# Kernel optimization log

Hardware: AMD Instinct MI355X
Metric: run time of the kernel (lower is better)

The kernel has to match this reference:

```python
import jax, jax.numpy as jnp
import numpy as np

N_ATOMS = 1000
BOX_L = 30.0      # cubic cell edge (Angstrom)
MAX_CUTOFF = 8.0  # max(cutoff)


def _np_cart(a, b, c):
    # numpy equivalent of torch.cartesian_prod for 3 1-D arrays
    g = np.meshgrid(a, b, c, indexing='ij')
    return np.stack(g, axis=-1).reshape(-1, 3)


def _np_get_shifts(cell, cutoff):
    # mirrors TorchNeighborListRangeSeparated._get_shifts (pbc=True on all axes)
    recip = np.linalg.inv(cell).T
    inv_len = np.linalg.norm(recip, axis=1)
    nrep = np.ceil(cutoff * inv_len).astype(np.int64)
    r1 = np.arange(1, nrep[0] + 1, dtype=np.float64)
    r2 = np.arange(1, nrep[1] + 1, dtype=np.float64)
    r3 = np.arange(1, nrep[2] + 1, dtype=np.float64)
    o = np.zeros(1, dtype=np.float64)
    return np.concatenate([
        _np_cart(r1, r2, r3), _np_cart(r1, r2, o), _np_cart(r1, r2, -r3),
        _np_cart(r1, o, r3), _np_cart(r1, o, o), _np_cart(r1, o, -r3),
        _np_cart(r1, -r2, r3), _np_cart(r1, -r2, o), _np_cart(r1, -r2, -r3),
        _np_cart(o, r2, r3), _np_cart(o, r2, o), _np_cart(o, r2, -r3),
        _np_cart(o, o, r3)], axis=0)


def setup_inputs() -> dict:
    key = jax.random.key(0)
    cell_np = np.eye(3) * BOX_L
    shifts = jnp.asarray(_np_get_shifts(cell_np, MAX_CUTOFF), dtype=jnp.float32)  # [13,3]
    positions = jax.random.uniform(key, (N_ATOMS, 3), dtype=jnp.float32) * BOX_L
    return {
        "positions": positions,
        "cell": jnp.asarray(cell_np, dtype=jnp.float32),
        "shifts": shifts,
        "cutoffs": jnp.array([4.0, 8.0], dtype=jnp.float32),
    }


def reference(positions, cell, shifts, cutoffs):
    """PBC-aware pairwise distance^2 + per-cutoff neighbor masks.

    Returns:
      d2:    [P] squared distances over all candidate pairs
             (N*(N-1)/2 in-cell pairs followed by S*N*N shifted-image pairs)
      masks: [n_cutoffs, P] int32 in-cutoff indicator (d2 < cutoff^2)
    """
    n = positions.shape[0]
    # in-cell pairs (torch.combinations -> i<j)
    iu, ju = jnp.triu_indices(n, k=1)
    rij_c = positions[iu] - positions[ju]                       # [Pc,3]
    d2_c = jnp.sum(rij_c * rij_c, axis=-1)                      # [Pc]
    # shifted-image pairs: all (shift, i, j)
    shift_values = shifts @ cell                                # [S,3]
    rij_o = (positions[None, :, None, :] - positions[None, None, :, :]
             + shift_values[:, None, None, :])                  # [S,N,N,3]
    d2_o = jnp.sum(rij_o * rij_o, axis=-1).reshape(-1)          # [S*N*N]
    d2 = jnp.concatenate([d2_c, d2_o], axis=0)                  # [P]
    masks = (d2[None, :] < (cutoffs ** 2)[:, None]).astype(jnp.int32)
    return d2, masks
```

## Files before the change

kernel.cpp:

```cpp
#include <hip/hip_runtime.h>
#include <math.h>


typedef float f32x4 __attribute__((ext_vector_type(4)));

template <int NCUT>
__global__ void __launch_bounds__(256) nbr_fast(
    const float* __restrict__ pos,
    const float* __restrict__ cell,
    const float* __restrict__ shifts,
    const float* __restrict__ cutoffs,
    int n, int S,
    float* __restrict__ out, unsigned P, unsigned Pc)
{
    const int tid = threadIdx.x;
    const int s   = blockIdx.z;

    double cut2[NCUT];
#pragma unroll
    for (int c = 0; c < NCUT; ++c) {
        double cv = (double)cutoffs[c];
        cut2[c] = cv * cv;
    }

    if (s < S) {
        const unsigned j0 = (unsigned)tid << 2;
        if (j0 >= (unsigned)n) return;
        const unsigned i = blockIdx.y;

        double s0 = (double)shifts[3*s+0], s1 = (double)shifts[3*s+1], s2 = (double)shifts[3*s+2];
        double sv0 = s0 * (double)cell[0] + s1 * (double)cell[3] + s2 * (double)cell[6];
        double sv1 = s0 * (double)cell[1] + s1 * (double)cell[4] + s2 * (double)cell[7];
        double sv2 = s0 * (double)cell[2] + s1 * (double)cell[5] + s2 * (double)cell[8];
        double pix = (double)pos[3*i+0];
        double piy = (double)pos[3*i+1];
        double piz = (double)pos[3*i+2];

        const float4* pj = (const float4*)(pos + 3 * j0);
        float4 a = pj[0], b = pj[1], c4 = pj[2];
        float jx[4] = {a.x, a.w, b.z, c4.y};
        float jy[4] = {a.y, b.x, b.w, c4.z};
        float jz[4] = {a.z, b.y, c4.x, c4.w};

        f32x4 d2v;
        f32x4 mv[NCUT];
#pragma unroll
        for (int k = 0; k < 4; ++k) {
            double dx = (pix - (double)jx[k]) + sv0;
            double dy = (piy - (double)jy[k]) + sv1;
            double dz = (piz - (double)jz[k]) + sv2;
            double d2 = dx*dx + dy*dy + dz*dz;
            d2v[k] = (float)d2;
#pragma unroll
            for (int c = 0; c < NCUT; ++c) mv[c][k] = (d2 < cut2[c]) ? 1.0f : 0.0f;
        }

        const unsigned t0 = ((unsigned)s * (unsigned)n + i) * (unsigned)n + j0 + Pc;
        *(f32x4*)(out + t0) = d2v;
#pragma unroll
        for (int c = 0; c < NCUT; ++c)
            *(f32x4*)(out + (unsigned)(c + 1) * P + t0) = mv[c];
    } else {
        const unsigned p0 = ((blockIdx.y * 256u) + (unsigned)tid) << 2;
        if (p0 >= Pc) return;

        const long long tn = 2LL * n - 1;
        f32x4 d2v;
        f32x4 mv[NCUT];
#pragma unroll
        for (int k = 0; k < 4; ++k) {
            long long p = (long long)p0 + k;
            double D = (double)(tn * tn) - 8.0 * (double)p;
            long long i = (long long)(((double)tn - sqrt(D)) * 0.5);
            if (i < 0) i = 0;
            if (i > n - 2) i = n - 2;
            while ((i + 1) * (tn - (i + 1)) / 2 <= p) ++i;
            while (i * (tn - i) / 2 > p) --i;
            long long j = p - i * (tn - i) / 2 + i + 1;

            double dx = (double)pos[3*i+0] - (double)pos[3*j+0];
            double dy = (double)pos[3*i+1] - (double)pos[3*j+1];
            double dz = (double)pos[3*i+2] - (double)pos[3*j+2];
            double d2 = dx*dx + dy*dy + dz*dz;
            d2v[k] = (float)d2;
#pragma unroll
            for (int c = 0; c < NCUT; ++c) mv[c][k] = (d2 < cut2[c]) ? 1.0f : 0.0f;
        }

        *(f32x4*)(out + p0) = d2v;
#pragma unroll
        for (int c = 0; c < NCUT; ++c)
            *(f32x4*)(out + (unsigned)(c + 1) * P + p0) = mv[c];
    }
}

__global__ void __launch_bounds__(256) nbr_scalar(
    const float* __restrict__ pos,
    const float* __restrict__ cell,
    const float* __restrict__ shifts,
    const float* __restrict__ cutoffs,
    int ncut, int n,
    float* __restrict__ out, long long P, long long Pc)
{
    long long p = (long long)blockIdx.x * 256 + threadIdx.x;
    if (p >= P) return;

    double d2;
    if (p >= Pc) {
        long long q = p - Pc;
        unsigned long long nn = (unsigned long long)n * n;
        unsigned s = (unsigned)(q / nn);
        unsigned long long r = q - (unsigned long long)s * nn;
        unsigned i = (unsigned)(r / n);
        unsigned j = (unsigned)(r - (unsigned long long)i * n);
        double s0 = (double)shifts[3*s+0], s1 = (double)shifts[3*s+1], s2 = (double)shifts[3*s+2];
        double sv0 = s0*(double)cell[0] + s1*(double)cell[3] + s2*(double)cell[6];
        double sv1 = s0*(double)cell[1] + s1*(double)cell[4] + s2*(double)cell[7];
        double sv2 = s0*(double)cell[2] + s1*(double)cell[5] + s2*(double)cell[8];
        double dx = ((double)pos[3*i+0] - (double)pos[3*j+0]) + sv0;
        double dy = ((double)pos[3*i+1] - (double)pos[3*j+1]) + sv1;
        double dz = ((double)pos[3*i+2] - (double)pos[3*j+2]) + sv2;
        d2 = dx*dx + dy*dy + dz*dz;
    } else {
        long long tn = 2LL * n - 1;
        double D = (double)(tn * tn) - 8.0 * (double)p;
        long long i = (long long)(((double)tn - sqrt(D)) * 0.5);
        if (i < 0) i = 0;
        if (i > n - 2) i = n - 2;
        while ((i + 1) * (tn - (i + 1)) / 2 <= p) ++i;
        while (i * (tn - i) / 2 > p) --i;
        long long j = p - i * (tn - i) / 2 + i + 1;
        double dx = (double)pos[3*i+0] - (double)pos[3*j+0];
        double dy = (double)pos[3*i+1] - (double)pos[3*j+1];
        double dz = (double)pos[3*i+2] - (double)pos[3*j+2];
        d2 = dx*dx + dy*dy + dz*dz;
    }
    out[p] = (float)d2;
    for (int c = 0; c < ncut; ++c) {
        double cv = (double)cutoffs[c];
        out[(long long)(c + 1) * P + p] = (d2 < cv * cv) ? 1.0f : 0.0f;
    }
}

extern "C" void kernel_launch(void* const* d_in, const int* in_sizes, int n_in,
                              void* d_out, int out_size, void* d_ws, size_t ws_size,
                              hipStream_t stream)
{
    const float* pos     = (const float*)d_in[0];
    const float* cell    = (const float*)d_in[1];
    const float* shifts  = (const float*)d_in[2];
    const float* cutoffs = (const float*)d_in[3];
    int n    = in_sizes[0] / 3;
    int S    = in_sizes[2] / 3;
    int ncut = in_sizes[3];

    long long Pc = (long long)n * (n - 1) / 2;
    long long P  = Pc + (long long)S * n * n;
    float* out = (float*)d_out;

    bool fast = ((n & 3) == 0) && (n <= 2049) && (ncut >= 1) && (ncut <= 4) &&
                (3 * P < (1LL << 31));
    if (fast) {
        dim3 grid(1, n, S + 1);
        unsigned uP = (unsigned)P, uPc = (unsigned)Pc;
        switch (ncut) {
        case 1: nbr_fast<1><<<grid, 256, 0, stream>>>(pos, cell, shifts, cutoffs, n, S, out, uP, uPc); break;
        case 2: nbr_fast<2><<<grid, 256, 0, stream>>>(pos, cell, shifts, cutoffs, n, S, out, uP, uPc); break;
        case 3: nbr_fast<3><<<grid, 256, 0, stream>>>(pos, cell, shifts, cutoffs, n, S, out, uP, uPc); break;
        default: nbr_fast<4><<<grid, 256, 0, stream>>>(pos, cell, shifts, cutoffs, n, S, out, uP, uPc); break;
        }
    } else {
        int blocks = (int)((P + 255) / 256);
        nbr_scalar<<<blocks, 256, 0, stream>>>(pos, cell, shifts, cutoffs,
                                               ncut, n, out, P, Pc);
    }
}
```

Baseline: 170.9 us.

## Replace 3D per-row grid with flat grid-stride loop over output chunks

Drops the grid of one block per (shift, i) row, where only part of each 256-thread block had work. Instead a fixed grid of up to 2048 blocks walks all 4-element output chunks with a grid-stride loop. Each chunk recovers its (shift, i, j) indices with integer division, or takes the triangular path for in-cell pairs. The aim is fully packed lanes and less block launch and scheduling overhead, at the price of per-chunk divisions and a mixed branch near the in-cell/shift boundary.

```diff
diff --git a/kernel.cpp b/kernel.cpp
--- a/kernel.cpp
+++ b/kernel.cpp
@@ -5,7 +5,7 @@
 typedef float f32x4 __attribute__((ext_vector_type(4)));
 
 template <int NCUT>
-__global__ void __launch_bounds__(256) nbr_fast(
+__global__ void __launch_bounds__(256) nbr_stride(
     const float* __restrict__ pos,
     const float* __restrict__ cell,
     const float* __restrict__ shifts,
@@ -13,78 +13,82 @@
     int n, int S,
     float* __restrict__ out, unsigned P, unsigned Pc)
 {
-    const int tid = threadIdx.x;
-    const int s   = blockIdx.z;
+    const unsigned Cs     = P >> 2;
+    const unsigned Ct     = Pc >> 2;
+    const unsigned stride = gridDim.x * blockDim.x;
+    unsigned u = blockIdx.x * blockDim.x + threadIdx.x;
 
+    const double c00 = cell[0], c01 = cell[1], c02 = cell[2];
+    const double c10 = cell[3], c11 = cell[4], c12 = cell[5];
+    const double c20 = cell[6], c21 = cell[7], c22 = cell[8];
     double cut2[NCUT];
 #pragma unroll
     for (int c = 0; c < NCUT; ++c) {
         double cv = (double)cutoffs[c];
         cut2[c] = cv * cv;
     }
+    const unsigned un = (unsigned)n;
+    const unsigned nn = un * un;
+    const long long tn = 2LL * n - 1;
 
-    if (s < S) {
-        const unsigned j0 = (unsigned)tid << 2;
-        if (j0 >= (unsigned)n) return;
-        const unsigned i = blockIdx.y;
-
-        double s0 = (double)shifts[3*s+0], s1 = (double)shifts[3*s+1], s2 = (double)shifts[3*s+2];
-        double sv0 = s0 * (double)cell[0] + s1 * (double)cell[3] + s2 * (double)cell[6];
-        double sv1 = s0 * (double)cell[1] + s1 * (double)cell[4] + s2 * (double)cell[7];
-        double sv2 = s0 * (double)cell[2] + s1 * (double)cell[5] + s2 * (double)cell[8];
-        double pix = (double)pos[3*i+0];
-        double piy = (double)pos[3*i+1];
-        double piz = (double)pos[3*i+2];
-
-        const float4* pj = (const float4*)(pos + 3 * j0);
-        float4 a = pj[0], b = pj[1], c4 = pj[2];
-        float jx[4] = {a.x, a.w, b.z, c4.y};
-        float jy[4] = {a.y, b.x, b.w, c4.z};
-        float jz[4] = {a.z, b.y, c4.x, c4.w};
-
+    for (; u < Cs; u += stride) {
+        const unsigned p0 = u << 2;
         f32x4 d2v;
         f32x4 mv[NCUT];
+
+        if (u >= Ct) {
+            const unsigned q  = p0 - Pc;
+            const unsigned s  = q / nn;
+            const unsigned r  = q - s * nn;
+            const unsigned i  = r / un;
+            const unsigned j0 = r - i * un;
+
+            const double s0 = (double)shifts[3*s+0];
+            const double s1 = (double)shifts[3*s+1];
+            const double s2 = (double)shifts[3*s+2];
+            const double sv0 = s0 * c00 + s1 * c10 + s2 * c20;
+            const double sv1 = s0 * c01 + s1 * c11 + s2 * c21;
+            const double sv2 = s0 * c02 + s1 * c12 + s2 * c22;
+            const double pix = (double)pos[3*i+0];
+            const double piy = (double)pos[3*i+1];
+            const double piz = (double)pos[3*i+2];
+
+            const float4* pj = (const float4*)(pos + 3 * j0);
+            float4 a = pj[0], b = pj[1], c4 = pj[2];
+            float jx[4] = {a.x, a.w, b.z, c4.y};
+            float jy[4] = {a.y, b.x, b.w, c4.z};
+            float jz[4] = {a.z, b.y, c4.x, c4.w};
+
 #pragma unroll
-        for (int k = 0; k < 4; ++k) {
-            double dx = (pix - (double)jx[k]) + sv0;
-            double dy = (piy - (double)jy[k]) + sv1;
-            double dz = (piz - (double)jz[k]) + sv2;
-            double d2 = dx*dx + dy*dy + dz*dz;
-            d2v[k] = (float)d2;
+            for (int k = 0; k < 4; ++k) {
+                double dx = (pix - (double)jx[k]) + sv0;
+                double dy = (piy - (double)jy[k]) + sv1;
+                double dz = (piz - (double)jz[k]) + sv2;
+                double d2 = dx*dx + dy*dy + dz*dz;
+                d2v[k] = (float)d2;
 #pragma unroll
-            for (int c = 0; c < NCUT; ++c) mv[c][k] = (d2 < cut2[c]) ? 1.0f : 0.0f;
-        }
+                for (int c = 0; c < NCUT; ++c) mv[c][k] = (d2 < cut2[c]) ? 1.0f : 0.0f;
+            }
+        } else {
+#pragma unroll
+            for (int k = 0; k < 4; ++k) {
+                long long p = (long long)p0 + k;
+                double D = (double)(tn * tn) - 8.0 * (double)p;
+                long long i = (long long)(((double)tn - sqrt(D)) * 0.5);
+                if (i < 0) i = 0;
+                if (i > n - 2) i = n - 2;
+                while ((i + 1) * (tn - (i + 1)) / 2 <= p) ++i;
+                while (i * (tn - i) / 2 > p) --i;
+                long long j = p - i * (tn - i) / 2 + i + 1;
 
-        const unsigned t0 = ((unsigned)s * (unsigned)n + i) * (unsigned)n + j0 + Pc;
-        *(f32x4*)(out + t0) = d2v;
+                double dx = (double)pos[3*i+0] - (double)pos[3*j+0];
+                double dy = (double)pos[3*i+1] - (double)pos[3*j+1];
+                double dz = (double)pos[3*i+2] - (double)pos[3*j+2];
+                double d2 = dx*dx + dy*dy + dz*dz;
+                d2v[k] = (float)d2;
 #pragma unroll
-        for (int c = 0; c < NCUT; ++c)
-            *(f32x4*)(out + (unsigned)(c + 1) * P + t0) = mv[c];
-    } else {
-        const unsigned p0 = ((blockIdx.y * 256u) + (unsigned)tid) << 2;
-        if (p0 >= Pc) return;
-
-        const long long tn = 2LL * n - 1;
-        f32x4 d2v;
-        f32x4 mv[NCUT];
-#pragma unroll
-        for (int k = 0; k < 4; ++k) {
-            long long p = (long long)p0 + k;
-            double D = (double)(tn * tn) - 8.0 * (double)p;
-            long long i = (long long)(((double)tn - sqrt(D)) * 0.5);
-            if (i < 0) i = 0;
-            if (i > n - 2) i = n - 2;
-            while ((i + 1) * (tn - (i + 1)) / 2 <= p) ++i;
-            while (i * (tn - i) / 2 > p) --i;
-            long long j = p - i * (tn - i) / 2 + i + 1;
-
-            double dx = (double)pos[3*i+0] - (double)pos[3*j+0];
-            double dy = (double)pos[3*i+1] - (double)pos[3*j+1];
-            double dz = (double)pos[3*i+2] - (double)pos[3*j+2];
-            double d2 = dx*dx + dy*dy + dz*dz;
-            d2v[k] = (float)d2;
-#pragma unroll
-            for (int c = 0; c < NCUT; ++c) mv[c][k] = (d2 < cut2[c]) ? 1.0f : 0.0f;
+                for (int c = 0; c < NCUT; ++c) mv[c][k] = (d2 < cut2[c]) ? 1.0f : 0.0f;
+            }
         }
 
         *(f32x4*)(out + p0) = d2v;
@@ -158,16 +162,19 @@
     long long P  = Pc + (long long)S * n * n;
     float* out = (float*)d_out;
 
-    bool fast = ((n & 3) == 0) && (n <= 2049) && (ncut >= 1) && (ncut <= 4) &&
+    bool fast = ((n & 3) == 0) && (ncut >= 1) && (ncut <= 4) &&
                 (3 * P < (1LL << 31));
     if (fast) {
-        dim3 grid(1, n, S + 1);
+        long long chunks = P >> 2;
+        int blocks = 2048;
+        long long need = (chunks + 255) / 256;
+        if (need < blocks) blocks = (int)need;
         unsigned uP = (unsigned)P, uPc = (unsigned)Pc;
         switch (ncut) {
-        case 1: nbr_fast<1><<<grid, 256, 0, stream>>>(pos, cell, shifts, cutoffs, n, S, out, uP, uPc); break;
-        case 2: nbr_fast<2><<<grid, 256, 0, stream>>>(pos, cell, shifts, cutoffs, n, S, out, uP, uPc); break;
-        case 3: nbr_fast<3><<<grid, 256, 0, stream>>>(pos, cell, shifts, cutoffs, n, S, out, uP, uPc); break;
-        default: nbr_fast<4><<<grid, 256, 0, stream>>>(pos, cell, shifts, cutoffs, n, S, out, uP, uPc); break;
+        case 1: nbr_stride<1><<<blocks, 256, 0, stream>>>(pos, cell, shifts, cutoffs, n, S, out, uP, uPc); break;
+        case 2: nbr_stride<2><<<blocks, 256, 0, stream>>>(pos, cell, shifts, cutoffs, n, S, out, uP, uPc); break;
+        case 3: nbr_stride<3><<<blocks, 256, 0, stream>>>(pos, cell, shifts, cutoffs, n, S, out, uP, uPc); break;
+        default: nbr_stride<4><<<blocks, 256, 0, stream>>>(pos, cell, shifts, cutoffs, n, S, out, uP, uPc); break;
         }
     } else {
         int blocks = (int)((P + 255) / 256);
```

New measurement: 171.2 us. Within noise of the previous version (+0.1%).
